# Kernel optimization log

Measured on AMD Instinct MI355X. Metric: run time of the kernel, lower is better.

## Reference

```python
import jax, jax.numpy as jnp
import numpy as np

N_ITERS = 1000  # hardcoded in the original module
EPS = 1e-6


def setup_inputs() -> dict:
    key = jax.random.key(0)
    k1, k2 = jax.random.split(key)
    embeds = jax.random.normal(k1, (30000, 64), dtype=jnp.float32)
    # torch does t.rand(...) inside forward; we hoist it here for determinism
    init_centroids = jax.random.uniform(k2, (500, 64), dtype=jnp.float32)
    return {"embeds": embeds, "init_centroids": init_centroids}


def reference(embeds, init_centroids):
    N, D = embeds.shape
    K = init_centroids.shape[0]
    # ||e||^2 is loop-invariant; squared L2 distance expanded as
    # ||e||^2 - 2 e.c + ||c||^2 (same math as (e-c)^2.sum(-1), no [N,K,D] blowup)
    e_sq = jnp.sum(embeds * embeds, axis=1)  # [N]
    ones = jnp.ones((N, 1), dtype=embeds.dtype)

    def step(carry, _):
        cents, _, _ = carry
        c_sq = jnp.sum(cents * cents, axis=1)  # [K]
        dists = e_sq[:, None] - 2.0 * (embeds @ cents.T) + c_sq[None, :]  # [N,K]
        idxs = jnp.argmin(dists, axis=1)  # [N] int32
        sums = jax.ops.segment_sum(embeds, idxs, num_segments=K)  # [K,D]
        counts = jax.ops.segment_sum(ones, idxs, num_segments=K)  # [K,1]
        new_cents = sums / (counts + EPS)
        return (new_cents, idxs, counts), None

    init = (init_centroids,
            jnp.zeros((N,), dtype=jnp.int32),
            jnp.zeros((K, 1), dtype=embeds.dtype))
    (centroids, idxs, clust_nums), _ = jax.lax.scan(step, init, None, length=N_ITERS)
    return centroids, idxs, clust_nums
```

## Files before the change

kernel.cpp:

```cpp
#include <hip/hip_runtime.h>
#include <math.h>

#define N_PTS   30000
#define DIM     64
#define K_C     500
#define K_PAD   512
#define N_ITERS 1000

#define GRID 256
#define BLK  512

#define TM    128
#define NTM   235
#define SA    132
#define SB    260
#define HALF  256

#define FPSCALE 262144.0f
#define INV_FPSCALE (1.0 / 262144.0)

#define SMEM_BYTES ((DIM * SA + DIM * SB) * 4 + (128 * 3 + 4) * 4)

#define BAR_STRIDE 32
#define BAR_REL_OFF (GRID * BAR_STRIDE)

__device__ __forceinline__ void gridbar(int* bar, int n) {
  __syncthreads();
  if (blockIdx.x == 0) {
    const int t = threadIdx.x;
    if (t >= 1 && t < GRID) {
      while (__hip_atomic_load(&bar[t * BAR_STRIDE], __ATOMIC_RELAXED,
                               __HIP_MEMORY_SCOPE_AGENT) < n)
        __builtin_amdgcn_s_sleep(2);
      __builtin_amdgcn_fence(__ATOMIC_ACQUIRE, "agent");
    }
    __syncthreads();
    if (t == 0)
      __hip_atomic_store(&bar[BAR_REL_OFF], n, __ATOMIC_RELEASE,
                         __HIP_MEMORY_SCOPE_AGENT);
  } else {
    if (threadIdx.x == 0) {
      __hip_atomic_store(&bar[blockIdx.x * BAR_STRIDE], n, __ATOMIC_RELEASE,
                         __HIP_MEMORY_SCOPE_AGENT);
      while (__hip_atomic_load(&bar[BAR_REL_OFF], __ATOMIC_RELAXED,
                               __HIP_MEMORY_SCOPE_AGENT) < n)
        __builtin_amdgcn_s_sleep(2);
      __builtin_amdgcn_fence(__ATOMIC_ACQUIRE, "agent");
    }
    __syncthreads();
  }
}

__global__ __launch_bounds__(BLK, 2)
void k_persist(const float* __restrict__ embeds,
               float* __restrict__ cents,
               float* __restrict__ csq,
               float* __restrict__ esq,
               int* __restrict__ idx,
               int* __restrict__ gcnt,
               unsigned long long* __restrict__ acc,
               float* __restrict__ cntf,
               int* __restrict__ changed,
               int* __restrict__ bar,
               float* __restrict__ out) {
  extern __shared__ __align__(16) char smem[];
  float (*As)[SA] = (float (*)[SA])smem;
  float (*Bs)[SB] = (float (*)[SB])(smem + DIM * SA * 4);
  int* bidxs   = (int*)(smem + (DIM * SA + DIM * SB) * 4);
  int* chg_pl  = bidxs + 128;
  int* chg_old = chg_pl + 128;
  int* chg_cnt = chg_old + 128;
  const int tid = threadIdx.x;
  const int bid = blockIdx.x;
  int bno = 0;

  {
    const int w = bid * 8 + (tid >> 6);
    const int d = tid & 63;
    for (int p = w; p < N_PTS; p += GRID * 8) {
      float v = embeds[(size_t)p * DIM + d];
      float s = v * v;
      #pragma unroll
      for (int m = 1; m < 64; m <<= 1) s += __shfl_xor(s, m, 64);
      if (d == 0) esq[p] = s;
    }
    if (w < K_PAD) {
      float v = (w < K_C) ? cents[(size_t)w * DIM + d] : 0.f;
      float s = v * v;
      #pragma unroll
      for (int m = 1; m < 64; m <<= 1) s += __shfl_xor(s, m, 64);
      if (d == 0) csq[w] = (w < K_C) ? s : INFINITY;
    }
  }
  gridbar(bar, ++bno);

  for (int it = 0; it < N_ITERS; ++it) {
    if (bid < NTM) {
      const int m0 = bid * TM;
      const int tx = tid & 31, ty = tid >> 5;
      if (tid == 0) chg_cnt[0] = 0;

      #pragma unroll
      for (int l = 0; l < 4; ++l) {
        int e = tid + l * BLK;
        int pl = e & 127, d4 = e >> 7;
        int p = m0 + pl;
        float4 v = make_float4(0.f, 0.f, 0.f, 0.f);
        if (p < N_PTS) v = *reinterpret_cast<const float4*>(embeds + (size_t)p * DIM + d4 * 4);
        As[d4 * 4 + 0][pl] = v.x; As[d4 * 4 + 1][pl] = v.y;
        As[d4 * 4 + 2][pl] = v.z; As[d4 * 4 + 3][pl] = v.w;
      }
      float esq_r[8];
      #pragma unroll
      for (int i = 0; i < 8; ++i) {
        int p = m0 + ty * 8 + i;
        esq_r[i] = (p < N_PTS) ? esq[p] : 0.f;
      }

      float best[8]; int bidx[8];
      #pragma unroll
      for (int i = 0; i < 8; ++i) { best[i] = INFINITY; bidx[i] = 0; }

      for (int h = 0; h < 2; ++h) {
        __syncthreads();
        #pragma unroll
        for (int l = 0; l < 8; ++l) {
          int e2 = tid + l * BLK;
          int kl = e2 & 255, d4 = e2 >> 8;
          float4 v = *reinterpret_cast<const float4*>(
              cents + (size_t)(h * HALF + kl) * DIM + d4 * 4);
          Bs[d4 * 4 + 0][kl] = v.x; Bs[d4 * 4 + 1][kl] = v.y;
          Bs[d4 * 4 + 2][kl] = v.z; Bs[d4 * 4 + 3][kl] = v.w;
        }
        __syncthreads();

        float acc_r[8][8];
        #pragma unroll
        for (int i = 0; i < 8; ++i)
          #pragma unroll
          for (int j = 0; j < 8; ++j) acc_r[i][j] = 0.f;

        #pragma unroll 8
        for (int d = 0; d < DIM; ++d) {
          float4 a0 = *reinterpret_cast<const float4*>(&As[d][ty * 8]);
          float4 a1 = *reinterpret_cast<const float4*>(&As[d][ty * 8 + 4]);
          float4 b0 = *reinterpret_cast<const float4*>(&Bs[d][tx * 4]);
          float4 b1 = *reinterpret_cast<const float4*>(&Bs[d][128 + tx * 4]);
          float av[8] = {a0.x, a0.y, a0.z, a0.w, a1.x, a1.y, a1.z, a1.w};
          float bv[8] = {b0.x, b0.y, b0.z, b0.w, b1.x, b1.y, b1.z, b1.w};
          #pragma unroll
          for (int i = 0; i < 8; ++i)
            #pragma unroll
            for (int j = 0; j < 8; ++j)
              acc_r[i][j] = fmaf(av[i], bv[j], acc_r[i][j]);
        }

        const int nbase = h * HALF;
        float4 c0 = *reinterpret_cast<const float4*>(&csq[nbase + tx * 4]);
        float4 c1 = *reinterpret_cast<const float4*>(&csq[nbase + 128 + tx * 4]);
        float cv[8] = {c0.x, c0.y, c0.z, c0.w, c1.x, c1.y, c1.z, c1.w};
        #pragma unroll
        for (int g = 0; g < 2; ++g) {
          #pragma unroll
          for (int j = 0; j < 4; ++j) {
            int c = g * 4 + j;
            int n = nbase + g * 128 + tx * 4 + j;
            #pragma unroll
            for (int i = 0; i < 8; ++i) {
              float dd = (esq_r[i] - 2.0f * acc_r[i][c]) + cv[c];
              if (dd < best[i]) { best[i] = dd; bidx[i] = n; }
            }
          }
        }
      }

      #pragma unroll
      for (int i = 0; i < 8; ++i) {
        float v = best[i]; int bi = bidx[i];
        #pragma unroll
        for (int s = 1; s < 32; s <<= 1) {
          float ov = __shfl_xor(v, s, 64);
          int   oi = __shfl_xor(bi, s, 64);
          if (ov < v || (ov == v && oi < bi)) { v = ov; bi = oi; }
        }
        if (tx == 0) {
          int pl = ty * 8 + i, p = m0 + pl;
          bidxs[pl] = bi;
          if (p < N_PTS) {
            int old = idx[p];
            if (old != bi) {
              idx[p] = bi;
              int slot = atomicAdd(chg_cnt, 1);
              chg_pl[slot] = pl;
              chg_old[slot] = old;
              if (slot == 0)
                __hip_atomic_store(&changed[it], 1, __ATOMIC_RELAXED,
                                   __HIP_MEMORY_SCOPE_AGENT);
            }
          }
        }
      }
      __syncthreads();

      {
        const int w = tid >> 6, lane = tid & 63;
        const int cnt = chg_cnt[0];
        for (int i = w; i < cnt; i += 8) {
          int pl = chg_pl[i];
          int old = chg_old[i];
          int k = bidxs[pl];
          float v = embeds[(size_t)(m0 + pl) * DIM + lane];
          long long iv = (long long)__float2int_rn(v * FPSCALE);
          atomicAdd(&acc[(size_t)k * DIM + lane], (unsigned long long)iv);
          if (old >= 0)
            atomicAdd(&acc[(size_t)old * DIM + lane], (unsigned long long)(-iv));
          if (lane == 0) {
            atomicAdd(&gcnt[k], 1);
            if (old >= 0) atomicAdd(&gcnt[old], -1);
          }
        }
      }
    }
    gridbar(bar, ++bno);

    if (__hip_atomic_load(&changed[it], __ATOMIC_RELAXED,
                          __HIP_MEMORY_SCOPE_AGENT) == 0)
      break;

    if (bid < (K_C + 7) / 8) {
      const int k = bid * 8 + (tid >> 6), d = tid & 63;
      if (k < K_C) {
        long long tot = (long long)acc[(size_t)k * DIM + d];
        int c = gcnt[k];
        float sum_f = (float)((double)tot * INV_FPSCALE);
        float nc = sum_f / ((float)c + 1e-6f);
        cents[(size_t)k * DIM + d] = nc;
        float sq = nc * nc;
        #pragma unroll
        for (int m = 1; m < 64; m <<= 1) sq += __shfl_xor(sq, m, 64);
        if (d == 0) { csq[k] = sq; cntf[k] = (float)c; }
      }
    }
    gridbar(bar, ++bno);
  }

  const int tot = K_C * DIM + N_PTS + K_C;
  for (int g = bid * BLK + tid; g < tot; g += GRID * BLK) {
    float v;
    if (g < K_C * DIM) v = cents[g];
    else if (g < K_C * DIM + N_PTS) v = (float)idx[g - K_C * DIM];
    else v = cntf[g - K_C * DIM - N_PTS];
    out[g] = v;
  }
}

extern "C" void kernel_launch(void* const* d_in, const int* in_sizes, int n_in,
                              void* d_out, int out_size, void* d_ws, size_t ws_size,
                              hipStream_t stream) {
  const float* embeds = (const float*)d_in[0];
  const float* init_c = (const float*)d_in[1];
  float* out = (float*)d_out;

  char* w = (char*)d_ws;
  size_t off = 0;
  auto alloc = [&](size_t bytes) -> void* {
    void* p = w + off;
    off += (bytes + 255) & ~(size_t)255;
    return p;
  };
  float* cents = (float*)alloc((size_t)K_PAD * DIM * sizeof(float));
  float* csq   = (float*)alloc((size_t)K_PAD * sizeof(float));
  float* esq   = (float*)alloc((size_t)N_PTS * sizeof(float));
  int*   idx   = (int*)  alloc((size_t)N_PTS * sizeof(int));
  float* cntf  = (float*)alloc((size_t)K_C * sizeof(float));
  int*   gcnt  = (int*)  alloc((size_t)K_C * sizeof(int));
  unsigned long long* acc =
      (unsigned long long*)alloc((size_t)K_C * DIM * sizeof(unsigned long long));
  int*   chg   = (int*)  alloc((size_t)N_ITERS * sizeof(int));
  int*   bar   = (int*)  alloc((size_t)(BAR_REL_OFF + 64) * sizeof(int));

  (void)hipFuncSetAttribute((const void*)k_persist,
                            hipFuncAttributeMaxDynamicSharedMemorySize, SMEM_BYTES);

  hipMemsetAsync(cents, 0, (size_t)K_PAD * DIM * sizeof(float), stream);
  hipMemcpyAsync(cents, init_c, (size_t)K_C * DIM * sizeof(float),
                 hipMemcpyDeviceToDevice, stream);
  hipMemsetAsync(gcnt, 0, (size_t)K_C * sizeof(int), stream);
  hipMemsetAsync(acc, 0, (size_t)K_C * DIM * sizeof(unsigned long long), stream);
  hipMemsetAsync(idx, 0xFF, (size_t)N_PTS * sizeof(int), stream);
  hipMemsetAsync(chg, 0, (size_t)N_ITERS * sizeof(int), stream);
  hipMemsetAsync(bar, 0, (size_t)(BAR_REL_OFF + 64) * sizeof(int), stream);

  k_persist<<<dim3(GRID), dim3(BLK), SMEM_BYTES, stream>>>(
      embeds, cents, csq, esq, idx, gcnt, acc, cntf, chg, bar, out);
}
```

Before: 2.091 ms.

## Add incremental k-means assignment that rescans only centroids that moved

Tracks which centroids changed each iteration (double-buffered mov flags and a dirty count). When few centroids moved, each point is compared only against the moved centroids using its cached best distance, and a full rescan is done only for points whose own centroid moved. The centroid update also skips unchanged clusters. This cuts the full N×K distance GEMM in late iterations, at the cost of extra global state, scalar per-thread dot products, and possible divergence from exact argmin semantics, since cached distances are reused while a point's centroid stays fixed.

```diff
diff --git a/kernel.cpp b/kernel.cpp
--- a/kernel.cpp
+++ b/kernel.cpp
@@ -15,6 +15,8 @@
 #define SA    132
 #define SB    260
 #define HALF  256
+
+#define DIRTY_MAX 96
 
 #define FPSCALE 262144.0f
 #define INV_FPSCALE (1.0 / 262144.0)
@@ -57,19 +59,27 @@
                float* __restrict__ csq,
                float* __restrict__ esq,
                int* __restrict__ idx,
+               float* __restrict__ db,
                int* __restrict__ gcnt,
                unsigned long long* __restrict__ acc,
                float* __restrict__ cntf,
+               int* __restrict__ mov,
+               int* __restrict__ dcnt_g,
                int* __restrict__ changed,
                int* __restrict__ bar,
                float* __restrict__ out) {
   extern __shared__ __align__(16) char smem[];
   float (*As)[SA] = (float (*)[SA])smem;
   float (*Bs)[SB] = (float (*)[SB])(smem + DIM * SA * 4);
-  int* bidxs   = (int*)(smem + (DIM * SA + DIM * SB) * 4);
-  int* chg_pl  = bidxs + 128;
-  int* chg_old = chg_pl + 128;
-  int* chg_cnt = chg_old + 128;
+  float* BsI    = (float*)(smem + DIM * SA * 4);
+  float* csqI   = BsI + DIRTY_MAX * 64;
+  int*   dlistL = (int*)(csqI + DIRTY_MAX);
+  int*   rl     = dlistL + DIRTY_MAX;
+  int*   rlc    = rl + 128;
+  int* ml_new  = (int*)(smem + (DIM * SA + DIM * SB) * 4);
+  int* ml_pl   = ml_new + 128;
+  int* ml_old  = ml_pl + 128;
+  int* ml_cnt  = ml_old + 128;
   const int tid = threadIdx.x;
   const int bid = blockIdx.x;
   int bno = 0;
@@ -95,10 +105,15 @@
   gridbar(bar, ++bno);
 
   for (int it = 0; it < N_ITERS; ++it) {
-    if (bid < NTM) {
+    int* mov_w = mov + (it & 1) * K_PAD;
+    int* mov_r = mov + ((it + 1) & 1) * K_PAD;
+    const int dprev = dcnt_g[(it + 1) & 1];
+    const bool use_inc = (it > 0) && (dprev <= DIRTY_MAX);
+
+    if (bid < NTM && !use_inc) {
       const int m0 = bid * TM;
       const int tx = tid & 31, ty = tid >> 5;
-      if (tid == 0) chg_cnt[0] = 0;
+      if (tid == 0) ml_cnt[0] = 0;
 
       #pragma unroll
       for (int l = 0; l < 4; ++l) {
@@ -185,14 +200,13 @@
         }
         if (tx == 0) {
           int pl = ty * 8 + i, p = m0 + pl;
-          bidxs[pl] = bi;
           if (p < N_PTS) {
+            db[p] = v;
             int old = idx[p];
             if (old != bi) {
               idx[p] = bi;
-              int slot = atomicAdd(chg_cnt, 1);
-              chg_pl[slot] = pl;
-              chg_old[slot] = old;
+              int slot = atomicAdd(ml_cnt, 1);
+              ml_pl[slot] = pl; ml_old[slot] = old; ml_new[slot] = bi;
               if (slot == 0)
                 __hip_atomic_store(&changed[it], 1, __ATOMIC_RELAXED,
                                    __HIP_MEMORY_SCOPE_AGENT);
@@ -204,11 +218,9 @@
 
       {
         const int w = tid >> 6, lane = tid & 63;
-        const int cnt = chg_cnt[0];
+        const int cnt = ml_cnt[0];
         for (int i = w; i < cnt; i += 8) {
-          int pl = chg_pl[i];
-          int old = chg_old[i];
-          int k = bidxs[pl];
+          int pl = ml_pl[i], old = ml_old[i], k = ml_new[i];
           float v = embeds[(size_t)(m0 + pl) * DIM + lane];
           long long iv = (long long)__float2int_rn(v * FPSCALE);
           atomicAdd(&acc[(size_t)k * DIM + lane], (unsigned long long)iv);
@@ -216,7 +228,134 @@
             atomicAdd(&acc[(size_t)old * DIM + lane], (unsigned long long)(-iv));
           if (lane == 0) {
             atomicAdd(&gcnt[k], 1);
-            if (old >= 0) atomicAdd(&gcnt[old], -1);
+            mov_w[k] = 1;
+            if (old >= 0) { atomicAdd(&gcnt[old], -1); mov_w[old] = 1; }
+          }
+        }
+      }
+    } else if (bid < NTM) {
+      const int m0 = bid * TM;
+      if (tid == 0) { ml_cnt[0] = 0; rlc[0] = 0; }
+
+      if (tid < 64) {
+        const int lane = tid;
+        int cnt8 = 0; int loc[8];
+        #pragma unroll
+        for (int c = 0; c < 8; ++c) {
+          int k = lane * 8 + c;
+          if (k < K_C && mov_r[k]) loc[cnt8++] = k;
+        }
+        int pre = cnt8;
+        #pragma unroll
+        for (int s = 1; s < 64; s <<= 1) {
+          int o = __shfl_up(pre, s, 64);
+          if (lane >= s) pre += o;
+        }
+        int excl = pre - cnt8;
+        for (int i = 0; i < cnt8; ++i) dlistL[excl + i] = loc[i];
+      }
+      #pragma unroll
+      for (int l = 0; l < 4; ++l) {
+        int e = tid + l * BLK;
+        int pl = e & 127, d4 = e >> 7;
+        int p = m0 + pl;
+        float4 v = make_float4(0.f, 0.f, 0.f, 0.f);
+        if (p < N_PTS) v = *reinterpret_cast<const float4*>(embeds + (size_t)p * DIM + d4 * 4);
+        As[d4 * 4 + 0][pl] = v.x; As[d4 * 4 + 1][pl] = v.y;
+        As[d4 * 4 + 2][pl] = v.z; As[d4 * 4 + 3][pl] = v.w;
+      }
+      __syncthreads();
+
+      for (int e = tid; e < dprev * 64; e += BLK) {
+        int jj = e >> 6, d = e & 63;
+        BsI[e] = cents[(size_t)dlistL[jj] * DIM + d];
+      }
+      for (int e = tid; e < dprev; e += BLK) csqI[e] = csq[dlistL[e]];
+      __syncthreads();
+
+      if (tid < TM) {
+        const int pl = tid, p = m0 + pl;
+        if (p < N_PTS) {
+          int k0 = idx[p];
+          if (mov_r[k0]) {
+            int s = atomicAdd(rlc, 1); rl[s] = pl;
+          } else {
+            float bestv = db[p]; int bi = k0;
+            float esq_p = esq[p];
+            for (int jj = 0; jj < dprev; ++jj) {
+              float dot = 0.f;
+              #pragma unroll 16
+              for (int d = 0; d < DIM; ++d)
+                dot = fmaf(As[d][pl], BsI[jj * 64 + d], dot);
+              float dd = (esq_p - 2.0f * dot) + csqI[jj];
+              int j = dlistL[jj];
+              if (dd < bestv || (dd == bestv && j < bi)) { bestv = dd; bi = j; }
+            }
+            if (bi != k0) {
+              idx[p] = bi; db[p] = bestv;
+              int s = atomicAdd(ml_cnt, 1);
+              ml_pl[s] = pl; ml_old[s] = k0; ml_new[s] = bi;
+              if (s == 0)
+                __hip_atomic_store(&changed[it], 1, __ATOMIC_RELAXED,
+                                   __HIP_MEMORY_SCOPE_AGENT);
+            }
+          }
+        }
+      }
+      __syncthreads();
+
+      {
+        const int w = tid >> 6, lane = tid & 63;
+        const int rcnt = rlc[0];
+        for (int i = w; i < rcnt; i += 8) {
+          int pl = rl[i], p = m0 + pl;
+          int k0 = idx[p];
+          float esq_p = esq[p];
+          float bestv = INFINITY; int bi = 0;
+          #pragma unroll
+          for (int c = 0; c < 8; ++c) {
+            int k = lane * 8 + c;
+            float dot = 0.f;
+            #pragma unroll 16
+            for (int d = 0; d < DIM; ++d)
+              dot = fmaf(As[d][pl], cents[(size_t)k * DIM + d], dot);
+            float dd = (esq_p - 2.0f * dot) + csq[k];
+            if (dd < bestv || (dd == bestv && k < bi)) { bestv = dd; bi = k; }
+          }
+          float v = bestv; int b2 = bi;
+          #pragma unroll
+          for (int s = 1; s < 64; s <<= 1) {
+            float ov = __shfl_xor(v, s, 64);
+            int   oi = __shfl_xor(b2, s, 64);
+            if (ov < v || (ov == v && oi < b2)) { v = ov; b2 = oi; }
+          }
+          if (lane == 0) {
+            db[p] = v;
+            if (b2 != k0) {
+              idx[p] = b2;
+              int s2 = atomicAdd(ml_cnt, 1);
+              ml_pl[s2] = pl; ml_old[s2] = k0; ml_new[s2] = b2;
+              if (s2 == 0)
+                __hip_atomic_store(&changed[it], 1, __ATOMIC_RELAXED,
+                                   __HIP_MEMORY_SCOPE_AGENT);
+            }
+          }
+        }
+      }
+      __syncthreads();
+
+      {
+        const int w = tid >> 6, lane = tid & 63;
+        const int cnt = ml_cnt[0];
+        for (int i = w; i < cnt; i += 8) {
+          int pl = ml_pl[i], old = ml_old[i], k = ml_new[i];
+          float v = embeds[(size_t)(m0 + pl) * DIM + lane];
+          long long iv = (long long)__float2int_rn(v * FPSCALE);
+          atomicAdd(&acc[(size_t)k * DIM + lane], (unsigned long long)iv);
+          atomicAdd(&acc[(size_t)old * DIM + lane], (unsigned long long)(-iv));
+          if (lane == 0) {
+            atomicAdd(&gcnt[k], 1);  atomicAdd(&gcnt[old], -1);
+            mov_w[k] = 1; mov_w[old] = 1;
           }
         }
       }
@@ -230,16 +369,27 @@
     if (bid < (K_C + 7) / 8) {
       const int k = bid * 8 + (tid >> 6), d = tid & 63;
       if (k < K_C) {
-        long long tot = (long long)acc[(size_t)k * DIM + d];
-        int c = gcnt[k];
-        float sum_f = (float)((double)tot * INV_FPSCALE);
-        float nc = sum_f / ((float)c + 1e-6f);
-        cents[(size_t)k * DIM + d] = nc;
-        float sq = nc * nc;
-        #pragma unroll
-        for (int m = 1; m < 64; m <<= 1) sq += __shfl_xor(sq, m, 64);
-        if (d == 0) { csq[k] = sq; cntf[k] = (float)c; }
-      }
+        const bool upd = (it == 0) || (mov_w[k] != 0);
+        if (upd) {
+          long long tot = (long long)acc[(size_t)k * DIM + d];
+          int c = gcnt[k];
+          float sum_f = (float)((double)tot * INV_FPSCALE);
+          float nc = sum_f / ((float)c + 1e-6f);
+          cents[(size_t)k * DIM + d] = nc;
+          float sq = nc * nc;
+          #pragma unroll
+          for (int m = 1; m < 64; m <<= 1) sq += __shfl_xor(sq, m, 64);
+          if (d == 0) {
+            csq[k] = sq; cntf[k] = (float)c;
+            if (it == 0) mov_w[k] = 1;
+            atomicAdd(&dcnt_g[it & 1], 1);
+          }
+        }
+      }
+    }
+    if (bid == 63) {
+      for (int e = tid; e < K_PAD; e += BLK) mov_r[e] = 0;
+      if (tid == 0) dcnt_g[(it + 1) & 1] = 0;
     }
     gridbar(bar, ++bno);
   }
@@ -272,10 +422,13 @@
   float* csq   = (float*)alloc((size_t)K_PAD * sizeof(float));
   float* esq   = (float*)alloc((size_t)N_PTS * sizeof(float));
   int*   idx   = (int*)  alloc((size_t)N_PTS * sizeof(int));
+  float* db    = (float*)alloc((size_t)N_PTS * sizeof(float));
   float* cntf  = (float*)alloc((size_t)K_C * sizeof(float));
   int*   gcnt  = (int*)  alloc((size_t)K_C * sizeof(int));
   unsigned long long* acc =
       (unsigned long long*)alloc((size_t)K_C * DIM * sizeof(unsigned long long));
+  int*   mov   = (int*)  alloc((size_t)2 * K_PAD * sizeof(int));
+  int*   dcnt  = (int*)  alloc((size_t)2 * sizeof(int));
   int*   chg   = (int*)  alloc((size_t)N_ITERS * sizeof(int));
   int*   bar   = (int*)  alloc((size_t)(BAR_REL_OFF + 64) * sizeof(int));
 
@@ -288,9 +441,11 @@
   hipMemsetAsync(gcnt, 0, (size_t)K_C * sizeof(int), stream);
   hipMemsetAsync(acc, 0, (size_t)K_C * DIM * sizeof(unsigned long long), stream);
   hipMemsetAsync(idx, 0xFF, (size_t)N_PTS * sizeof(int), stream);
+  hipMemsetAsync(mov, 0, (size_t)2 * K_PAD * sizeof(int), stream);
+  hipMemsetAsync(dcnt, 0, (size_t)2 * sizeof(int), stream);
   hipMemsetAsync(chg, 0, (size_t)N_ITERS * sizeof(int), stream);
   hipMemsetAsync(bar, 0, (size_t)(BAR_REL_OFF + 64) * sizeof(int), stream);
 
   k_persist<<<dim3(GRID), dim3(BLK), SMEM_BYTES, stream>>>(
-      embeds, cents, csq, esq, idx, gcnt, acc, cntf, chg, bar, out);
+      embeds, cents, csq, esq, idx, db, gcnt, acc, cntf, mov, dcnt, chg, bar, out);
 }
```

New measurement: 3.819 ms. 1.83x slower.

## Recompute centroids per block from accumulators, dropping second grid barrier

Applied to the files above, without the earlier changes.

Each block now rebuilds all 512 centroids and their squared norms from the fixed-point accumulators and counts at the start of each iteration, rather than a subset of blocks writing centroids to global memory behind a second grid barrier. This halves the grid-wide barriers per iteration. It also holds all centroids in LDS (no padding) and widens the per-thread register tile to 8x16, replacing the two half passes. In exchange, every block redundantly reads the full accumulator array each iteration and does divides and double conversions. The larger LDS footprint and 128 accumulators per thread may cut occupancy or cause bank conflicts.

```diff
diff --git a/kernel.cpp b/kernel.cpp
--- a/kernel.cpp
+++ b/kernel.cpp
@@ -12,14 +12,11 @@
 
 #define TM    128
 #define NTM   235
-#define SA    132
-#define SB    260
-#define HALF  256
 
 #define FPSCALE 262144.0f
 #define INV_FPSCALE (1.0 / 262144.0)
 
-#define SMEM_BYTES ((DIM * SA + DIM * SB) * 4 + (128 * 3 + 4) * 4)
+#define SMEM_BYTES (DIM * TM * 4 + DIM * K_PAD * 4)
 
 #define BAR_STRIDE 32
 #define BAR_REL_OFF (GRID * BAR_STRIDE)
@@ -53,30 +50,28 @@
 
 __global__ __launch_bounds__(BLK, 2)
 void k_persist(const float* __restrict__ embeds,
-               float* __restrict__ cents,
-               float* __restrict__ csq,
+               const float* __restrict__ cents0,
                float* __restrict__ esq,
                int* __restrict__ idx,
                int* __restrict__ gcnt,
                unsigned long long* __restrict__ acc,
-               float* __restrict__ cntf,
                int* __restrict__ changed,
                int* __restrict__ bar,
                float* __restrict__ out) {
   extern __shared__ __align__(16) char smem[];
-  float (*As)[SA] = (float (*)[SA])smem;
-  float (*Bs)[SB] = (float (*)[SB])(smem + DIM * SA * 4);
-  int* bidxs   = (int*)(smem + (DIM * SA + DIM * SB) * 4);
-  int* chg_pl  = bidxs + 128;
-  int* chg_old = chg_pl + 128;
-  int* chg_cnt = chg_old + 128;
+  float* As = (float*)smem;
+  float* Bs = (float*)(smem + DIM * TM * 4);
+  float* csqL   = (float*)smem;
+  int*   ml_new = (int*)(smem + 2048);
+  int*   ml_pl  = (int*)(smem + 2560);
+  int*   ml_old = (int*)(smem + 3072);
+  int*   ml_cnt = (int*)(smem + 3584);
   const int tid = threadIdx.x;
   const int bid = blockIdx.x;
   int bno = 0;
 
   {
-    const int w = bid * 8 + (tid >> 6);
-    const int d = tid & 63;
+    const int w = bid * 8 + (tid >> 6), d = tid & 63;
     for (int p = w; p < N_PTS; p += GRID * 8) {
       float v = embeds[(size_t)p * DIM + d];
       float s = v * v;
@@ -84,22 +79,20 @@
       for (int m = 1; m < 64; m <<= 1) s += __shfl_xor(s, m, 64);
       if (d == 0) esq[p] = s;
     }
-    if (w < K_PAD) {
-      float v = (w < K_C) ? cents[(size_t)w * DIM + d] : 0.f;
-      float s = v * v;
-      #pragma unroll
-      for (int m = 1; m < 64; m <<= 1) s += __shfl_xor(s, m, 64);
-      if (d == 0) csq[w] = (w < K_C) ? s : INFINITY;
-    }
   }
   gridbar(bar, ++bno);
+
+  const int m0 = bid * TM;
+  const int tx = tid & 31, ty = tid >> 5;
+  float esq_r[8];
+  #pragma unroll
+  for (int i = 0; i < 8; ++i) {
+    int p = m0 + ty * 8 + i;
+    esq_r[i] = (p < N_PTS) ? esq[p] : 0.f;
+  }
 
   for (int it = 0; it < N_ITERS; ++it) {
     if (bid < NTM) {
-      const int m0 = bid * TM;
-      const int tx = tid & 31, ty = tid >> 5;
-      if (tid == 0) chg_cnt[0] = 0;
-
       #pragma unroll
       for (int l = 0; l < 4; ++l) {
         int e = tid + l * BLK;
@@ -107,69 +100,101 @@
         int p = m0 + pl;
         float4 v = make_float4(0.f, 0.f, 0.f, 0.f);
         if (p < N_PTS) v = *reinterpret_cast<const float4*>(embeds + (size_t)p * DIM + d4 * 4);
-        As[d4 * 4 + 0][pl] = v.x; As[d4 * 4 + 1][pl] = v.y;
-        As[d4 * 4 + 2][pl] = v.z; As[d4 * 4 + 3][pl] = v.w;
-      }
-      float esq_r[8];
-      #pragma unroll
-      for (int i = 0; i < 8; ++i) {
-        int p = m0 + ty * 8 + i;
-        esq_r[i] = (p < N_PTS) ? esq[p] : 0.f;
-      }
+        As[(d4 * 4 + 0) * TM + pl] = v.x; As[(d4 * 4 + 1) * TM + pl] = v.y;
+        As[(d4 * 4 + 2) * TM + pl] = v.z; As[(d4 * 4 + 3) * TM + pl] = v.w;
+      }
+
+      float csq_reg;
+      {
+        float s4[16];
+        if (it == 0) {
+          #pragma unroll
+          for (int l = 0; l < 16; ++l) {
+            float4 v = *reinterpret_cast<const float4*>(cents0 + (size_t)tid * DIM + l * 4);
+            Bs[(l * 4 + 0) * K_PAD + tid] = v.x; Bs[(l * 4 + 1) * K_PAD + tid] = v.y;
+            Bs[(l * 4 + 2) * K_PAD + tid] = v.z; Bs[(l * 4 + 3) * K_PAD + tid] = v.w;
+            s4[l] = (v.x * v.x + v.y * v.y) + (v.z * v.z + v.w * v.w);
+          }
+        } else if (tid < K_C) {
+          float fc = (float)gcnt[tid] + 1e-6f;
+          #pragma unroll
+          for (int l = 0; l < 16; ++l) {
+            const unsigned long long* ap = acc + (size_t)tid * DIM + l * 4;
+            longlong2 a0 = *reinterpret_cast<const longlong2*>(ap);
+            longlong2 a1 = *reinterpret_cast<const longlong2*>(ap + 2);
+            float n0 = (float)((double)a0.x * INV_FPSCALE) / fc;
+            float n1 = (float)((double)a0.y * INV_FPSCALE) / fc;
+            float n2 = (float)((double)a1.x * INV_FPSCALE) / fc;
+            float n3 = (float)((double)a1.y * INV_FPSCALE) / fc;
+            Bs[(l * 4 + 0) * K_PAD + tid] = n0; Bs[(l * 4 + 1) * K_PAD + tid] = n1;
+            Bs[(l * 4 + 2) * K_PAD + tid] = n2; Bs[(l * 4 + 3) * K_PAD + tid] = n3;
+            s4[l] = (n0 * n0 + n1 * n1) + (n2 * n2 + n3 * n3);
+          }
+        } else {
+          #pragma unroll
+          for (int l = 0; l < 16; ++l) {
+            Bs[(l * 4 + 0) * K_PAD + tid] = 0.f; Bs[(l * 4 + 1) * K_PAD + tid] = 0.f;
+            Bs[(l * 4 + 2) * K_PAD + tid] = 0.f; Bs[(l * 4 + 3) * K_PAD + tid] = 0.f;
+            s4[l] = 0.f;
+          }
+        }
+        float s8[8], s16[4], s32[2];
+        #pragma unroll
+        for (int m = 0; m < 8; ++m) s8[m] = s4[2 * m] + s4[2 * m + 1];
+        #pragma unroll
+        for (int m = 0; m < 4; ++m) s16[m] = s8[2 * m] + s8[2 * m + 1];
+        s32[0] = s16[0] + s16[1]; s32[1] = s16[2] + s16[3];
+        csq_reg = s32[0] + s32[1];
+        if (tid >= K_C) csq_reg = INFINITY;
+      }
+      __syncthreads();
+
+      float acc_r[8][16];
+      #pragma unroll
+      for (int i = 0; i < 8; ++i)
+        #pragma unroll
+        for (int j = 0; j < 16; ++j) acc_r[i][j] = 0.f;
+
+      #pragma unroll 4
+      for (int d = 0; d < DIM; ++d) {
+        const float* ar = As + d * TM + ty * 8;
+        float4 a0 = *reinterpret_cast<const float4*>(ar);
+        float4 a1 = *reinterpret_cast<const float4*>(ar + 4);
+        const float* br = Bs + d * K_PAD + tx * 4;
+        float4 b0 = *reinterpret_cast<const float4*>(br);
+        float4 b1 = *reinterpret_cast<const float4*>(br + 128);
+        float4 b2 = *reinterpret_cast<const float4*>(br + 256);
+        float4 b3 = *reinterpret_cast<const float4*>(br + 384);
+        float av[8]  = {a0.x, a0.y, a0.z, a0.w, a1.x, a1.y, a1.z, a1.w};
+        float bv[16] = {b0.x, b0.y, b0.z, b0.w, b1.x, b1.y, b1.z, b1.w,
+                        b2.x, b2.y, b2.z, b2.w, b3.x, b3.y, b3.z, b3.w};
+        #pragma unroll
+        for (int i = 0; i < 8; ++i)
+          #pragma unroll
+          for (int j = 0; j < 16; ++j)
+            acc_r[i][j] = fmaf(av[i], bv[j], acc_r[i][j]);
+      }
+
+      __syncthreads();
+      csqL[tid] = csq_reg;
+      if (tid == 0) ml_cnt[0] = 0;
+      __syncthreads();
 
       float best[8]; int bidx[8];
       #pragma unroll
       for (int i = 0; i < 8; ++i) { best[i] = INFINITY; bidx[i] = 0; }
-
-      for (int h = 0; h < 2; ++h) {
-        __syncthreads();
-        #pragma unroll
-        for (int l = 0; l < 8; ++l) {
-          int e2 = tid + l * BLK;
-          int kl = e2 & 255, d4 = e2 >> 8;
-          float4 v = *reinterpret_cast<const float4*>(
-              cents + (size_t)(h * HALF + kl) * DIM + d4 * 4);
-          Bs[d4 * 4 + 0][kl] = v.x; Bs[d4 * 4 + 1][kl] = v.y;
-          Bs[d4 * 4 + 2][kl] = v.z; Bs[d4 * 4 + 3][kl] = v.w;
-        }
-        __syncthreads();
-
-        float acc_r[8][8];
-        #pragma unroll
-        for (int i = 0; i < 8; ++i)
-          #pragma unroll
-          for (int j = 0; j < 8; ++j) acc_r[i][j] = 0.f;
-
-        #pragma unroll 8
-        for (int d = 0; d < DIM; ++d) {
-          float4 a0 = *reinterpret_cast<const float4*>(&As[d][ty * 8]);
-          float4 a1 = *reinterpret_cast<const float4*>(&As[d][ty * 8 + 4]);
-          float4 b0 = *reinterpret_cast<const float4*>(&Bs[d][tx * 4]);
-          float4 b1 = *reinterpret_cast<const float4*>(&Bs[d][128 + tx * 4]);
-          float av[8] = {a0.x, a0.y, a0.z, a0.w, a1.x, a1.y, a1.z, a1.w};
-          float bv[8] = {b0.x, b0.y, b0.z, b0.w, b1.x, b1.y, b1.z, b1.w};
-          #pragma unroll
-          for (int i = 0; i < 8; ++i)
-            #pragma unroll
-            for (int j = 0; j < 8; ++j)
-              acc_r[i][j] = fmaf(av[i], bv[j], acc_r[i][j]);
-        }
-
-        const int nbase = h * HALF;
-        float4 c0 = *reinterpret_cast<const float4*>(&csq[nbase + tx * 4]);
-        float4 c1 = *reinterpret_cast<const float4*>(&csq[nbase + 128 + tx * 4]);
-        float cv[8] = {c0.x, c0.y, c0.z, c0.w, c1.x, c1.y, c1.z, c1.w};
-        #pragma unroll
-        for (int g = 0; g < 2; ++g) {
-          #pragma unroll
-          for (int j = 0; j < 4; ++j) {
-            int c = g * 4 + j;
-            int n = nbase + g * 128 + tx * 4 + j;
-            #pragma unroll
-            for (int i = 0; i < 8; ++i) {
-              float dd = (esq_r[i] - 2.0f * acc_r[i][c]) + cv[c];
-              if (dd < best[i]) { best[i] = dd; bidx[i] = n; }
-            }
+      #pragma unroll
+      for (int q = 0; q < 4; ++q) {
+        float4 cq = *reinterpret_cast<const float4*>(csqL + q * 128 + tx * 4);
+        float cv[4] = {cq.x, cq.y, cq.z, cq.w};
+        #pragma unroll
+        for (int j = 0; j < 4; ++j) {
+          int c = q * 4 + j;
+          int n = q * 128 + tx * 4 + j;
+          #pragma unroll
+          for (int i = 0; i < 8; ++i) {
+            float dd = (esq_r[i] - 2.0f * acc_r[i][c]) + cv[j];
+            if (dd < best[i]) { best[i] = dd; bidx[i] = n; }
           }
         }
       }
@@ -185,14 +210,12 @@
         }
         if (tx == 0) {
           int pl = ty * 8 + i, p = m0 + pl;
-          bidxs[pl] = bi;
           if (p < N_PTS) {
             int old = idx[p];
             if (old != bi) {
               idx[p] = bi;
-              int slot = atomicAdd(chg_cnt, 1);
-              chg_pl[slot] = pl;
-              chg_old[slot] = old;
+              int slot = atomicAdd(ml_cnt, 1);
+              ml_pl[slot] = pl; ml_old[slot] = old; ml_new[slot] = bi;
               if (slot == 0)
                 __hip_atomic_store(&changed[it], 1, __ATOMIC_RELAXED,
                                    __HIP_MEMORY_SCOPE_AGENT);
@@ -203,12 +226,10 @@
       __syncthreads();
 
       {
-        const int w = tid >> 6, lane = tid & 63;
-        const int cnt = chg_cnt[0];
-        for (int i = w; i < cnt; i += 8) {
-          int pl = chg_pl[i];
-          int old = chg_old[i];
-          int k = bidxs[pl];
+        const int w8 = tid >> 6, lane = tid & 63;
+        const int cnt = ml_cnt[0];
+        for (int i = w8; i < cnt; i += 8) {
+          int pl = ml_pl[i], old = ml_old[i], k = ml_new[i];
           float v = embeds[(size_t)(m0 + pl) * DIM + lane];
           long long iv = (long long)__float2int_rn(v * FPSCALE);
           atomicAdd(&acc[(size_t)k * DIM + lane], (unsigned long long)iv);
@@ -226,30 +247,19 @@
     if (__hip_atomic_load(&changed[it], __ATOMIC_RELAXED,
                           __HIP_MEMORY_SCOPE_AGENT) == 0)
       break;
-
-    if (bid < (K_C + 7) / 8) {
-      const int k = bid * 8 + (tid >> 6), d = tid & 63;
-      if (k < K_C) {
-        long long tot = (long long)acc[(size_t)k * DIM + d];
-        int c = gcnt[k];
-        float sum_f = (float)((double)tot * INV_FPSCALE);
-        float nc = sum_f / ((float)c + 1e-6f);
-        cents[(size_t)k * DIM + d] = nc;
-        float sq = nc * nc;
-        #pragma unroll
-        for (int m = 1; m < 64; m <<= 1) sq += __shfl_xor(sq, m, 64);
-        if (d == 0) { csq[k] = sq; cntf[k] = (float)c; }
-      }
-    }
-    gridbar(bar, ++bno);
   }
 
   const int tot = K_C * DIM + N_PTS + K_C;
   for (int g = bid * BLK + tid; g < tot; g += GRID * BLK) {
     float v;
-    if (g < K_C * DIM) v = cents[g];
-    else if (g < K_C * DIM + N_PTS) v = (float)idx[g - K_C * DIM];
-    else v = cntf[g - K_C * DIM - N_PTS];
+    if (g < K_C * DIM) {
+      int k = g >> 6;
+      v = (float)((double)(long long)acc[g] * INV_FPSCALE) / ((float)gcnt[k] + 1e-6f);
+    } else if (g < K_C * DIM + N_PTS) {
+      v = (float)idx[g - K_C * DIM];
+    } else {
+      v = (float)gcnt[g - K_C * DIM - N_PTS];
+    }
     out[g] = v;
   }
 }
@@ -268,22 +278,20 @@
     off += (bytes + 255) & ~(size_t)255;
     return p;
   };
-  float* cents = (float*)alloc((size_t)K_PAD * DIM * sizeof(float));
-  float* csq   = (float*)alloc((size_t)K_PAD * sizeof(float));
-  float* esq   = (float*)alloc((size_t)N_PTS * sizeof(float));
-  int*   idx   = (int*)  alloc((size_t)N_PTS * sizeof(int));
-  float* cntf  = (float*)alloc((size_t)K_C * sizeof(float));
-  int*   gcnt  = (int*)  alloc((size_t)K_C * sizeof(int));
+  float* cents0 = (float*)alloc((size_t)K_PAD * DIM * sizeof(float));
+  float* esq    = (float*)alloc((size_t)N_PTS * sizeof(float));
+  int*   idx    = (int*)  alloc((size_t)N_PTS * sizeof(int));
+  int*   gcnt   = (int*)  alloc((size_t)K_C * sizeof(int));
   unsigned long long* acc =
       (unsigned long long*)alloc((size_t)K_C * DIM * sizeof(unsigned long long));
-  int*   chg   = (int*)  alloc((size_t)N_ITERS * sizeof(int));
-  int*   bar   = (int*)  alloc((size_t)(BAR_REL_OFF + 64) * sizeof(int));
+  int*   chg    = (int*)  alloc((size_t)N_ITERS * sizeof(int));
+  int*   bar    = (int*)  alloc((size_t)(BAR_REL_OFF + 64) * sizeof(int));
 
   (void)hipFuncSetAttribute((const void*)k_persist,
                             hipFuncAttributeMaxDynamicSharedMemorySize, SMEM_BYTES);
 
-  hipMemsetAsync(cents, 0, (size_t)K_PAD * DIM * sizeof(float), stream);
-  hipMemcpyAsync(cents, init_c, (size_t)K_C * DIM * sizeof(float),
+  hipMemsetAsync(cents0, 0, (size_t)K_PAD * DIM * sizeof(float), stream);
+  hipMemcpyAsync(cents0, init_c, (size_t)K_C * DIM * sizeof(float),
                  hipMemcpyDeviceToDevice, stream);
   hipMemsetAsync(gcnt, 0, (size_t)K_C * sizeof(int), stream);
   hipMemsetAsync(acc, 0, (size_t)K_C * DIM * sizeof(unsigned long long), stream);
@@ -292,5 +300,5 @@
   hipMemsetAsync(bar, 0, (size_t)(BAR_REL_OFF + 64) * sizeof(int), stream);
 
   k_persist<<<dim3(GRID), dim3(BLK), SMEM_BYTES, stream>>>(
-      embeds, cents, csq, esq, idx, gcnt, acc, cntf, chg, bar, out);
+      embeds, cents0, esq, idx, gcnt, acc, chg, bar, out);
 }
```

Measured after the change: 1.944 ms. 7.0% less time.
